# Kernel tuning notes

Hardware: AMD Instinct MI355X
Metric: run time of the kernel (lower is better)

Reference implementation:

```python
import jax, jax.numpy as jnp
import numpy as np
from jax import lax

SEQ_LEN = 256
INPUT_DIM = 1
HIDDEN = 1024
NUM_CLASSES = 10
BATCH = 512


def _kaiming_uniform(key, shape):
    # torch kaiming_uniform_ default: bound = sqrt(6 / fan_in), fan_in = shape[1]
    fan_in = shape[1]
    bound = float(np.sqrt(6.0 / fan_in))
    return jax.random.uniform(key, shape, jnp.float32, -bound, bound)


def setup_inputs() -> dict:
    key = jax.random.key(0)
    ks = jax.random.split(key, 16)
    inp = {"x": jax.random.normal(ks[0], (BATCH, SEQ_LEN), jnp.float32)}
    names_shapes = [
        ("Wgx", (HIDDEN, INPUT_DIM)), ("Wgh", (HIDDEN, HIDDEN)), ("bg", (HIDDEN, 1)),
        ("Wix", (HIDDEN, INPUT_DIM)), ("Wih", (HIDDEN, HIDDEN)), ("bi", (HIDDEN, 1)),
        ("Wfx", (HIDDEN, INPUT_DIM)), ("Wfh", (HIDDEN, HIDDEN)), ("bf", (HIDDEN, 1)),
        ("Wox", (HIDDEN, INPUT_DIM)), ("Woh", (HIDDEN, HIDDEN)), ("bo", (HIDDEN, 1)),
        ("Wph", (NUM_CLASSES, HIDDEN)), ("bp", (NUM_CLASSES, 1)),
    ]
    for k, (name, shape) in zip(ks[1:], names_shapes):
        inp[name] = _kaiming_uniform(k, shape)
    return inp


def reference(x, Wgx, Wgh, bg, Wix, Wih, bi, Wfx, Wfh, bf, Wox, Woh, bo, Wph, bp):
    B = x.shape[0]
    H = Wgh.shape[0]
    h0 = jnp.zeros((H, B), x.dtype)
    c0 = jnp.zeros((H, B), x.dtype)
    xs = x.T  # [S, B]; each step xt is [B] (input_dim == 1)

    def step(carry, xt):
        ht, ct = carry
        xt = xt[None, :]  # [1, B]
        g = jnp.tanh(Wgx @ xt + Wgh @ ht + bg)
        i = jax.nn.sigmoid(Wix @ xt + Wih @ ht + bi)
        f = jax.nn.sigmoid(Wfx @ xt + Wfh @ ht + bf)
        o = jax.nn.sigmoid(Wox @ xt + Woh @ ht + bo)
        ct = g * i + ct * f
        ht = jnp.tanh(ct) * o
        return (ht, ct), None

    (ht, ct), _ = lax.scan(step, (h0, c0), xs)
    pt = Wph @ ht + bp  # [num_classes, B], only last step's pt is returned
    return pt.T  # [B, num_classes]
```

## Files before the change

### kernel.cpp

```cpp
#include <hip/hip_runtime.h>


#define HID  1024
#define SEQL 256

typedef __bf16 bf16x8 __attribute__((ext_vector_type(8)));
typedef float  f32x16 __attribute__((ext_vector_type(16)));
typedef unsigned u32x4 __attribute__((ext_vector_type(4)));

#define AS1 __attribute__((address_space(1)))
#define AS3 __attribute__((address_space(3)))

__device__ __forceinline__ float fast_sigmoid(float v) {
    float e = __expf(-v);
    return 1.0f / (1.0f + e);
}
__device__ __forceinline__ float fast_tanh(float v) {
    float e = __expf(2.0f * v);
    return 1.0f - 2.0f / (e + 1.0f);
}
__device__ __forceinline__ unsigned pk2bf(float a, float b) {
    unsigned short ua = __builtin_bit_cast(unsigned short, (__bf16)a);
    unsigned short ub = __builtin_bit_cast(unsigned short, (__bf16)b);
    return (unsigned)ua | ((unsigned)ub << 16);
}
__device__ __forceinline__ float bfhi(unsigned u) { return __builtin_bit_cast(float, u & 0xFFFF0000u); }
__device__ __forceinline__ float bflo(unsigned u) { return __builtin_bit_cast(float, u << 16); }

__device__ __forceinline__ u32x4 load16_sc1(const void* p) {
    u32x4 r;
    asm volatile("global_load_dwordx4 %0, %1, off sc1\n\t"
                 "s_waitcnt vmcnt(0)"
                 : "=v"(r) : "v"(p) : "memory");
    return r;
}

__global__ __launch_bounds__(256) void lstm_init(unsigned short* htA, unsigned* cnt, float* out) {
    int idx = blockIdx.x * 256 + threadIdx.x;
    uint4 z; z.x = 0; z.y = 0; z.z = 0; z.w = 0;
    ((uint4*)htA)[idx] = z;
    if (idx < 512) cnt[idx] = 0;
    if (idx < 5120) out[idx] = 0.05f;
}

__global__ __attribute__((amdgpu_flat_work_group_size(256, 256), amdgpu_waves_per_eu(1, 1)))
void lstm_main(
    const float* __restrict__ x,
    const float* __restrict__ Wgx, const float* __restrict__ Wgh, const float* __restrict__ bg,
    const float* __restrict__ Wix, const float* __restrict__ Wih, const float* __restrict__ bi,
    const float* __restrict__ Wfx, const float* __restrict__ Wfh, const float* __restrict__ bf_,
    const float* __restrict__ Wox, const float* __restrict__ Woh, const float* __restrict__ bo,
    const float* __restrict__ Wph, const float* __restrict__ bp,
    float* __restrict__ out,
    unsigned short* __restrict__ htA, unsigned short* __restrict__ htB,
    unsigned* __restrict__ cnt)
{
    __shared__ uint4 ldsB[2][16][2][64];

    const int tid = threadIdx.x;
    const int w   = tid >> 6;
    const int l   = tid & 63;
    const int l31 = l & 31;
    const int h5  = l >> 5;
    const int gid = blockIdx.x;
    const int c   = gid & 7;
    const int r   = gid >> 3;

    const int gate = l31 >> 3;
    const int hrow = (r << 5) + (w << 3) + (l & 7);
    const float* Wsel = (gate == 0) ? Wgh : (gate == 1) ? Wih : (gate == 2) ? Wfh : Woh;
    const float* wrow = Wsel + hrow * HID + (h5 << 3);
    bf16x8 A[64];
#pragma unroll
    for (int kk = 0; kk < 64; ++kk) {
        const float4* p = (const float4*)(wrow + kk * 16);
        float4 u0 = p[0], u1 = p[1];
        bf16x8 a;
        a[0] = (__bf16)u0.x; a[1] = (__bf16)u0.y; a[2] = (__bf16)u0.z; a[3] = (__bf16)u0.w;
        a[4] = (__bf16)u1.x; a[5] = (__bf16)u1.y; a[6] = (__bf16)u1.z; a[7] = (__bf16)u1.w;
        A[kk] = a;
        __builtin_amdgcn_sched_barrier(0);
    }

    float wx16[16], bs16[16];
    {
        const float* WxA[4] = {Wgx, Wix, Wfx, Wox};
        const float* bA[4]  = {bg, bi, bf_, bo};
#pragma unroll
        for (int j = 0; j < 16; ++j) {
            int g = j >> 2;
            int h = (r << 5) + (w << 3) + (j & 3) + (h5 << 2);
            wx16[j] = WxA[g][h];
            bs16[j] = bA[g][h];
        }
    }

    float ct[8];
#pragma unroll
    for (int i = 0; i < 8; ++i) ct[i] = 0.f;

    const unsigned short* htR = htA;
    unsigned short*       htW = htB;
    unsigned* mycnt = cnt + (c << 6);

    for (int t = 0; t < SEQL; ++t) {
        float xv0 = x[(unsigned)((c << 6) + l31) * SEQL + (unsigned)t];
        float xv1 = x[(unsigned)((c << 6) + 32 + l31) * SEQL + (unsigned)t];

        const unsigned short* gR = htR + (c << 16);

#pragma unroll
        for (int j = 0; j < 8; ++j) {
            int q = (w << 3) + j;
            const void* g = (const void*)(gR + q * 512 + (l << 3));
            __builtin_amdgcn_global_load_lds((const AS1 void*)g,
                (AS3 void*)&ldsB[0][q >> 1][q & 1][0], 16, 0, 0x10 );
        }

        f32x16 acc0, acc1;
#pragma unroll
        for (int j = 0; j < 16; ++j) {
            acc0[j] = fmaf(wx16[j], xv0, bs16[j]);
            acc1[j] = fmaf(wx16[j], xv1, bs16[j]);
        }

#pragma unroll
        for (int ch = 0; ch < 4; ++ch) {
            if (ch < 3) {
#pragma unroll
                for (int j = 0; j < 8; ++j) {
                    int q = (w << 3) + j;
                    const void* g = (const void*)(gR + (ch + 1) * 16384 + q * 512 + (l << 3));
                    __builtin_amdgcn_global_load_lds((const AS1 void*)g,
                        (AS3 void*)&ldsB[(ch + 1) & 1][q >> 1][q & 1][0], 16, 0, 0x10 );
                }
                asm volatile("s_waitcnt vmcnt(8)" ::: "memory");
            } else {
                asm volatile("s_waitcnt vmcnt(0)" ::: "memory");
            }
            __builtin_amdgcn_s_barrier();
            asm volatile("" ::: "memory");
#pragma unroll
            for (int kk = 0; kk < 16; ++kk) {
                bf16x8 b0 = __builtin_bit_cast(bf16x8, ldsB[ch & 1][kk][0][l]);
                bf16x8 b1 = __builtin_bit_cast(bf16x8, ldsB[ch & 1][kk][1][l]);
                acc0 = __builtin_amdgcn_mfma_f32_32x32x16_bf16(A[ch * 16 + kk], b0, acc0, 0, 0, 0);
                acc1 = __builtin_amdgcn_mfma_f32_32x32x16_bf16(A[ch * 16 + kk], b1, acc1, 0, 0, 0);
            }
            asm volatile("" ::: "memory");
            __builtin_amdgcn_s_barrier();
        }

        float htv[8];
#pragma unroll
        for (int nt = 0; nt < 2; ++nt) {
            f32x16 ac = nt ? acc1 : acc0;
#pragma unroll
            for (int d = 0; d < 4; ++d) {
                float g  = fast_tanh(ac[d]);
                float ii = fast_sigmoid(ac[4 + d]);
                float ff = fast_sigmoid(ac[8 + d]);
                float oo = fast_sigmoid(ac[12 + d]);
                float cc = fmaf(ct[nt * 4 + d], ff, g * ii);
                ct[nt * 4 + d] = cc;
                htv[nt * 4 + d] = fast_tanh(cc) * oo;
            }
        }

        {
            unsigned short* gW = htW + (c << 16);
            int kkw  = (r << 1) + (w >> 1);
            int slot = ((w & 1) << 5) + l31;
#pragma unroll
            for (int nt = 0; nt < 2; ++nt) {
                unsigned lo = pk2bf(htv[nt * 4 + 0], htv[nt * 4 + 1]);
                unsigned hi = pk2bf(htv[nt * 4 + 2], htv[nt * 4 + 3]);
                unsigned long long v = (unsigned long long)lo | ((unsigned long long)hi << 32);
                unsigned long long* dst =
                    (unsigned long long*)(gW + (((kkw * 2 + nt) * 64 + slot) * 8 + (h5 << 2)));
                __hip_atomic_store(dst, v, __ATOMIC_RELAXED, __HIP_MEMORY_SCOPE_AGENT);
            }
        }

        __syncthreads();
        if (tid == 0) {
            __hip_atomic_fetch_add(mycnt, 1u, __ATOMIC_RELAXED, __HIP_MEMORY_SCOPE_AGENT);
            unsigned tgt = 32u * (unsigned)(t + 1);
            while (__hip_atomic_load(mycnt, __ATOMIC_RELAXED, __HIP_MEMORY_SCOPE_AGENT) < tgt) {
                __builtin_amdgcn_s_sleep(1);
            }
        }
        __syncthreads();

        const unsigned short* tmp = htR; htR = htW; htW = (unsigned short*)tmp;
    }

    {
        const unsigned short* hfin = htR + (c << 16);
        for (int p = w; p < 20; p += 4) {
            int bloc = (r << 1) + (p / 10);
            int bb   = (c << 6) + bloc;
            int cls  = p % 10;
            const unsigned short* base = hfin + l * 1024 + ((bloc >> 5) & 1) * 512
                                              + (bloc & 31) * 8;
            u32x4 u0 = load16_sc1(base);
            u32x4 u1 = load16_sc1(base + 256);
            const float* wp = Wph + (unsigned)cls * HID + (unsigned)l * 16;
            float s = 0.f;
#pragma unroll
            for (int e = 0; e < 4; ++e) {
                s = fmaf(wp[2 * e],         bflo(u0[e]), s);
                s = fmaf(wp[2 * e + 1],     bfhi(u0[e]), s);
                s = fmaf(wp[8 + 2 * e],     bflo(u1[e]), s);
                s = fmaf(wp[8 + 2 * e + 1], bfhi(u1[e]), s);
            }
#pragma unroll
            for (int off = 32; off > 0; off >>= 1) s += __shfl_xor(s, off, 64);
            if (l == 0) out[bb * 10 + cls] = s + bp[cls];
        }
    }
}

extern "C" void kernel_launch(void* const* d_in, const int* in_sizes, int n_in,
                              void* d_out, int out_size, void* d_ws, size_t ws_size,
                              hipStream_t stream) {
    const float* x   = (const float*)d_in[0];
    const float* Wgx = (const float*)d_in[1];
    const float* Wgh = (const float*)d_in[2];
    const float* bg  = (const float*)d_in[3];
    const float* Wix = (const float*)d_in[4];
    const float* Wih = (const float*)d_in[5];
    const float* bi  = (const float*)d_in[6];
    const float* Wfx = (const float*)d_in[7];
    const float* Wfh = (const float*)d_in[8];
    const float* bf_ = (const float*)d_in[9];
    const float* Wox = (const float*)d_in[10];
    const float* Woh = (const float*)d_in[11];
    const float* bo  = (const float*)d_in[12];
    const float* Wph = (const float*)d_in[13];
    const float* bp  = (const float*)d_in[14];
    float* out = (float*)d_out;

    char* ws = (char*)d_ws;
    unsigned short* htA = (unsigned short*)ws;
    unsigned short* htB = (unsigned short*)(ws + (1 << 20));
    unsigned*       cnt = (unsigned*)(ws + (2 << 20));

    lstm_init<<<dim3(256), dim3(256), 0, stream>>>(htA, cnt, out);

    lstm_main<<<dim3(256), dim3(256), 0, stream>>>(
        x, Wgx, Wgh, bg, Wix, Wih, bi, Wfx, Wfh, bf_,
        Wox, Woh, bo, Wph, bp, out, htA, htB, cnt);
}
```

Measured before the change: 2.131 ms.

## Replace atomic counter barrier with per-block flags, full-step LDS prefetch

Swaps the shared atomic fetch-add grid barrier for per-block flag stores that a whole wavefront polls and checks with a ballot, which removes contended atomics on a single counter. It also issues all four chunks of the h-state load into a 128KB dynamic LDS buffer at once, so the per-chunk trailing barriers and double-buffer reuse go away. The next step's x values are prefetched. This raises LDS use to 128KB per block and adds 64 polling lanes per block on the flag array.

```diff
diff --git a/kernel.cpp b/kernel.cpp
--- a/kernel.cpp
+++ b/kernel.cpp
@@ -35,11 +35,11 @@
     return r;
 }
 
-__global__ __launch_bounds__(256) void lstm_init(unsigned short* htA, unsigned* cnt, float* out) {
+__global__ __launch_bounds__(256) void lstm_init(unsigned short* htA, unsigned* flags, float* out) {
     int idx = blockIdx.x * 256 + threadIdx.x;
     uint4 z; z.x = 0; z.y = 0; z.z = 0; z.w = 0;
     ((uint4*)htA)[idx] = z;
-    if (idx < 512) cnt[idx] = 0;
+    if (idx < 512) flags[idx] = 0;
     if (idx < 5120) out[idx] = 0.05f;
 }
 
@@ -53,9 +53,9 @@
     const float* __restrict__ Wph, const float* __restrict__ bp,
     float* __restrict__ out,
     unsigned short* __restrict__ htA, unsigned short* __restrict__ htB,
-    unsigned* __restrict__ cnt)
+    unsigned* __restrict__ flags)
 {
-    __shared__ uint4 ldsB[2][16][2][64];
+    extern __shared__ uint4 ldsB[];
 
     const int tid = threadIdx.x;
     const int w   = tid >> 6;
@@ -101,21 +101,29 @@
 
     const unsigned short* htR = htA;
     unsigned short*       htW = htB;
-    unsigned* mycnt = cnt + (c << 6);
+    unsigned* gflags = flags + (c << 6);
+    const float* xrow0 = x + (unsigned)((c << 6) + l31) * SEQL;
+    const float* xrow1 = x + (unsigned)((c << 6) + 32 + l31) * SEQL;
+
+    float xv0 = xrow0[0], xv1 = xrow1[0];
 
     for (int t = 0; t < SEQL; ++t) {
-        float xv0 = x[(unsigned)((c << 6) + l31) * SEQL + (unsigned)t];
-        float xv1 = x[(unsigned)((c << 6) + 32 + l31) * SEQL + (unsigned)t];
-
         const unsigned short* gR = htR + (c << 16);
 
 #pragma unroll
-        for (int j = 0; j < 8; ++j) {
-            int q = (w << 3) + j;
-            const void* g = (const void*)(gR + q * 512 + (l << 3));
-            __builtin_amdgcn_global_load_lds((const AS1 void*)g,
-                (AS3 void*)&ldsB[0][q >> 1][q & 1][0], 16, 0, 0x10 );
-        }
+        for (int ch = 0; ch < 4; ++ch) {
+#pragma unroll
+            for (int j = 0; j < 8; ++j) {
+                int q = (w << 3) + j;
+                const void* g = (const void*)(gR + ch * 16384 + q * 512 + (l << 3));
+                __builtin_amdgcn_global_load_lds((const AS1 void*)g,
+                    (AS3 void*)&ldsB[(ch * 32 + q) * 64], 16, 0, 0x10 );
+            }
+        }
+        __builtin_amdgcn_sched_barrier(0);
+        int tn = (t + 1 < SEQL) ? t + 1 : t;
+        float nx0 = xrow0[tn], nx1 = xrow1[tn];
+        __builtin_amdgcn_sched_barrier(0);
 
         f32x16 acc0, acc1;
 #pragma unroll
@@ -126,29 +134,19 @@
 
 #pragma unroll
         for (int ch = 0; ch < 4; ++ch) {
-            if (ch < 3) {
-#pragma unroll
-                for (int j = 0; j < 8; ++j) {
-                    int q = (w << 3) + j;
-                    const void* g = (const void*)(gR + (ch + 1) * 16384 + q * 512 + (l << 3));
-                    __builtin_amdgcn_global_load_lds((const AS1 void*)g,
-                        (AS3 void*)&ldsB[(ch + 1) & 1][q >> 1][q & 1][0], 16, 0, 0x10 );
-                }
-                asm volatile("s_waitcnt vmcnt(8)" ::: "memory");
-            } else {
-                asm volatile("s_waitcnt vmcnt(0)" ::: "memory");
-            }
+            if      (ch == 0) asm volatile("s_waitcnt vmcnt(24)" ::: "memory");
+            else if (ch == 1) asm volatile("s_waitcnt vmcnt(16)" ::: "memory");
+            else if (ch == 2) asm volatile("s_waitcnt vmcnt(8)"  ::: "memory");
+            else              asm volatile("s_waitcnt vmcnt(2)"  ::: "memory");
             __builtin_amdgcn_s_barrier();
             asm volatile("" ::: "memory");
 #pragma unroll
             for (int kk = 0; kk < 16; ++kk) {
-                bf16x8 b0 = __builtin_bit_cast(bf16x8, ldsB[ch & 1][kk][0][l]);
-                bf16x8 b1 = __builtin_bit_cast(bf16x8, ldsB[ch & 1][kk][1][l]);
+                bf16x8 b0 = __builtin_bit_cast(bf16x8, ldsB[(ch * 32 + kk * 2 + 0) * 64 + l]);
+                bf16x8 b1 = __builtin_bit_cast(bf16x8, ldsB[(ch * 32 + kk * 2 + 1) * 64 + l]);
                 acc0 = __builtin_amdgcn_mfma_f32_32x32x16_bf16(A[ch * 16 + kk], b0, acc0, 0, 0, 0);
                 acc1 = __builtin_amdgcn_mfma_f32_32x32x16_bf16(A[ch * 16 + kk], b1, acc1, 0, 0, 0);
             }
-            asm volatile("" ::: "memory");
-            __builtin_amdgcn_s_barrier();
         }
 
         float htv[8];
@@ -182,16 +180,22 @@
             }
         }
 
+        asm volatile("s_waitcnt vmcnt(0)" ::: "memory");
         __syncthreads();
-        if (tid == 0) {
-            __hip_atomic_fetch_add(mycnt, 1u, __ATOMIC_RELAXED, __HIP_MEMORY_SCOPE_AGENT);
-            unsigned tgt = 32u * (unsigned)(t + 1);
-            while (__hip_atomic_load(mycnt, __ATOMIC_RELAXED, __HIP_MEMORY_SCOPE_AGENT) < tgt) {
+        unsigned target = (unsigned)(t + 1);
+        if (tid == 0)
+            __hip_atomic_store(&gflags[r], target, __ATOMIC_RELAXED, __HIP_MEMORY_SCOPE_AGENT);
+        if (w == 0) {
+            const unsigned* fp = gflags + l31;
+            while (true) {
+                unsigned v = __hip_atomic_load(fp, __ATOMIC_RELAXED, __HIP_MEMORY_SCOPE_AGENT);
+                if (__ballot(v >= target) == ~0ull) break;
                 __builtin_amdgcn_s_sleep(1);
             }
         }
         __syncthreads();
 
+        xv0 = nx0; xv1 = nx1;
         const unsigned short* tmp = htR; htR = htW; htW = (unsigned short*)tmp;
     }
 
@@ -244,11 +248,17 @@
     char* ws = (char*)d_ws;
     unsigned short* htA = (unsigned short*)ws;
     unsigned short* htB = (unsigned short*)(ws + (1 << 20));
-    unsigned*       cnt = (unsigned*)(ws + (2 << 20));
-
-    lstm_init<<<dim3(256), dim3(256), 0, stream>>>(htA, cnt, out);
-
-    lstm_main<<<dim3(256), dim3(256), 0, stream>>>(
+    unsigned*     flags = (unsigned*)(ws + (2 << 20));
+
+    lstm_init<<<dim3(256), dim3(256), 0, stream>>>(htA, flags, out);
+
+    static int lds_set = 0;
+    if (!lds_set) {
+        hipFuncSetAttribute((const void*)lstm_main,
+                            hipFuncAttributeMaxDynamicSharedMemorySize, 131072);
+        lds_set = 1;
+    }
+    lstm_main<<<dim3(256), dim3(256), 131072, stream>>>(
         x, Wgx, Wgh, bg, Wix, Wih, bi, Wfx, Wfh, bf_,
-        Wox, Woh, bo, Wph, bp, out, htA, htB, cnt);
-}
+        Wox, Woh, bo, Wph, bp, out, htA, htB, flags);
+}
```

Measured after the change: 2.142 ms. Within noise of the previous version (+0.5%).
